# Optimization experiments

Hardware: AMD Instinct MI355X
Metric: run time of the kernel (lower is better)

## Reference

```python
import jax, jax.numpy as jnp
from jax import lax
import numpy as np

C = 768      # embed_dim
H = 8        # num_heads
SR = 2       # sr_ratio
EPS = 1e-5


def setup_inputs() -> dict:
    key = jax.random.key(0)
    ks = jax.random.split(key, 8)
    B, n = 1, 24
    N = n ** 3  # 13824
    s = 0.02
    x = jax.random.normal(ks[0], (B, N, C), jnp.float32)
    wq = jax.random.normal(ks[1], (C, C), jnp.float32) * s          # query (no bias)
    wkv = jax.random.normal(ks[2], (C, 2 * C), jnp.float32) * s     # key_value (no bias)
    sr_w = jax.random.normal(ks[3], (C, C, SR, SR, SR), jnp.float32) * s  # Conv3d OIDHW
    sr_b = jax.random.normal(ks[4], (C,), jnp.float32) * s
    ln_g = jnp.ones((C,), jnp.float32)
    ln_b = jnp.zeros((C,), jnp.float32)
    proj_w = jax.random.normal(ks[5], (C, C), jnp.float32) * s
    proj_b = jax.random.normal(ks[6], (C,), jnp.float32) * s
    return {"x": x, "wq": wq, "wkv": wkv, "sr_w": sr_w, "sr_b": sr_b,
            "ln_g": ln_g, "ln_b": ln_b, "proj_w": proj_w, "proj_b": proj_b}


def reference(x, wq, wkv, sr_w, sr_b, ln_g, ln_b, proj_w, proj_b):
    B, N, Cdim = x.shape
    d = Cdim // H
    n = round(N ** (1.0 / 3.0))
    # q: [B,H,N,d]
    q = (x @ wq).reshape(B, N, H, d).transpose(0, 2, 1, 3)
    # spatial reduction: conv3d with kernel=stride=SR
    x_ = x.transpose(0, 2, 1).reshape(B, Cdim, n, n, n)
    x_ = lax.conv_general_dilated(x_, sr_w, (SR, SR, SR), 'VALID',
                                  dimension_numbers=('NCDHW', 'OIDHW', 'NCDHW'))
    x_ = x_ + sr_b[None, :, None, None, None]
    x_ = x_.reshape(B, Cdim, -1).transpose(0, 2, 1)  # [B, N', C]
    mu = x_.mean(-1, keepdims=True)
    var = x_.var(-1, keepdims=True)
    x_ = (x_ - mu) / jnp.sqrt(var + EPS) * ln_g + ln_b
    # kv: [2,B,H,N',d]
    kv = (x_ @ wkv).reshape(B, -1, 2, H, d).transpose(2, 0, 3, 1, 4)
    k, v = kv[0], kv[1]
    # NOTE: original scales by sqrt(num_heads), not sqrt(head_dim) -- kept faithfully.
    scores = jnp.einsum('bhqd,bhkd->bhqk', q, k) / jnp.sqrt(jnp.float32(H))
    probs = jax.nn.softmax(scores, axis=-1)
    out = jnp.einsum('bhqk,bhkd->bhqd', probs, v)
    out = out.transpose(0, 2, 1, 3).reshape(B, N, Cdim)
    return out @ proj_w + proj_b
```

## Files before the change

kernel.cpp:

```cpp
#include <hip/hip_runtime.h>
#include <hip/hip_bf16.h>

typedef __hip_bfloat16 bf16;
typedef unsigned short u16;

#define CD 768
#define HH 8
#define HD 96
#define NT 13824
#define NR 1728
#define KCONV 6144
#define NRCD 1327104L

typedef __attribute__((ext_vector_type(8))) __bf16 bf16x8;
typedef __attribute__((ext_vector_type(8))) unsigned short us8;
typedef __attribute__((ext_vector_type(4))) unsigned short us4;
typedef __attribute__((ext_vector_type(4))) float floatx4;

#define OFF_XB   0L
#define OFF_Q    21233664L
#define OFF_XR   42467328L
#define OFF_XLN  47775744L
#define OFF_WQT  50429952L
#define OFF_WKVT 51609600L
#define OFF_PRJT 53968896L
#define OFF_SRWR 55148544L
#define OFF_PRB  64587264L

__device__ __forceinline__ float b2f(bf16 v) { return __bfloat162float(v); }
__device__ __forceinline__ floatx4 mfma16(bf16x8 a, bf16x8 b, floatx4 c) {
    return __builtin_amdgcn_mfma_f32_16x16x32_bf16(a, b, c, 0, 0, 0);
}
__device__ __forceinline__ u16 f2bf_bits(float x) {
    return __builtin_bit_cast(u16, __float2bfloat16(x));
}
__device__ __forceinline__ float ldin(const void* p, long i, int bf) {
    return bf ? b2f(((const bf16*)p)[i]) : ((const float*)p)[i];
}
__device__ __forceinline__ int probe_bf(const void* lng) {
    return ((const u16*)lng)[0] == 0x3F80;
}

#define GLOAD16(gp, lp) __builtin_amdgcn_global_load_lds( \
    (const __attribute__((address_space(1))) unsigned int*)(gp), \
    (__attribute__((address_space(3))) unsigned int*)(lp), 16, 0, 0)

__device__ __forceinline__ void do_trans(
    const void* __restrict__ src, bf16* __restrict__ dst, int R, int Cc,
    int bf, int bx32, int by32, int tx, int ty, float (*tile)[33])
{
    const int bx = bx32 * 32, by = by32 * 32;
#pragma unroll
    for (int rr = 0; rr < 4; ++rr)
        tile[ty + rr * 8][tx] = ldin(src, (long)(by + ty + rr * 8) * Cc + bx + tx, bf);
    __syncthreads();
#pragma unroll
    for (int rr = 0; rr < 4; ++rr)
        dst[(long)(bx + ty + rr * 8) * R + by + tx] =
            __float2bfloat16(tile[tx][ty + rr * 8]);
}

__global__ __launch_bounds__(256) void prep_kernel(
    const void* __restrict__ wq, const void* __restrict__ wkv,
    const void* __restrict__ proj_w, const void* __restrict__ sr_w,
    const void* __restrict__ proj_b, const void* __restrict__ x,
    const void* __restrict__ lng,
    bf16* __restrict__ wqT, bf16* __restrict__ wkvT, bf16* __restrict__ prjT,
    bf16* __restrict__ srwR, bf16* __restrict__ prbB, bf16* __restrict__ xb)
{
    __shared__ float tile[32][33];
    const int bf = probe_bf(lng);
    const int tx = threadIdx.x & 31, ty = threadIdx.x >> 5;
    const int id = blockIdx.x;
    if (id < 576) {
        do_trans(wq, wqT, CD, CD, bf, id % 24, id / 24, tx, ty, tile);
    } else if (id < 1728) {
        int j = id - 576;
        do_trans(wkv, wkvT, CD, 1536, bf, j % 48, j / 48, tx, ty, tile);
    } else if (id < 2304) {
        int j = id - 1728;
        do_trans(proj_w, prjT, CD, CD, bf, j % 24, j / 24, tx, ty, tile);
    } else if (id < 3456) {
        int j = id - 2304;
        const long total = 768L * 6144;
        for (long e = (long)j * 256 + threadIdx.x; e < total; e += 1152L * 256) {
            long o = e / 6144;
            int rem = (int)(e - o * 6144);
            int tap = rem / 768, i = rem - tap * 768;
            srwR[e] = __float2bfloat16(ldin(sr_w, o * 6144 + i * 8 + tap, bf));
        }
    } else if (id == 3456) {
        if (threadIdx.x < 96) {
            long c = threadIdx.x;
            if (bf) {
                ((us8*)prbB)[c] = ((const us8*)proj_b)[c];
            } else {
                const float* s = (const float*)proj_b + c * 8;
                us8 o;
#pragma unroll
                for (int jj = 0; jj < 8; ++jj) o[jj] = f2bf_bits(s[jj]);
                ((us8*)prbB)[c] = o;
            }
        }
    } else {
        long c = (long)(id - 3457) * 256 + threadIdx.x;
        if (c < (long)NT * CD / 8) {
            if (bf) {
                ((us8*)xb)[c] = ((const us8*)x)[c];
            } else {
                const float* s = (const float*)x + c * 8;
                us8 o;
#pragma unroll
                for (int jj = 0; jj < 8; ++jj) o[jj] = f2bf_bits(s[jj]);
                ((us8*)xb)[c] = o;
            }
        }
    }
}

template <bool GATHER, bool BIAS, int DST, int SPLITK, bool PRESCALE>
__device__ __forceinline__ void gemm_body(
    const bf16* __restrict__ A, const bf16* __restrict__ Bt,
    const bf16* __restrict__ bias, void* __restrict__ C, bf16* __restrict__ C2,
    int M, int N, int K, const void* __restrict__ lng,
    int bidx, int bidy, int bidz,
    u16 (*__restrict__ Al)[128][32], u16 (*__restrict__ Bl)[128][32])
{
    const int tid  = threadIdx.x;
    const int wave = tid >> 6, lane = tid & 63;
    const int l15  = lane & 15, quad = lane >> 4;
    const int m0 = bidy * 128, n0 = bidx * 128;
    const int mw = (wave & 1) * 64, nw = (wave >> 1) * 64;

    const int row0 = wave * 16 + (lane >> 2);
    const int row1 = row0 + 64;
    const int cb8  = (((lane & 3) ^ ((lane >> 3) & 3)) << 3);

    int tokbase0 = 0, tokbase1 = 0;
    long arow0 = 0, arow1 = 0;
    {
        int mc0 = min(m0 + row0, M - 1);
        int mc1 = min(m0 + row1, M - 1);
        if (GATHER) {
            int zo0 = mc0 / 144, yo0 = (mc0 / 12) % 12, xo0 = mc0 % 12;
            tokbase0 = zo0 * 1152 + yo0 * 48 + xo0 * 2;
            int zo1 = mc1 / 144, yo1 = (mc1 / 12) % 12, xo1 = mc1 % 12;
            tokbase1 = zo1 * 1152 + yo1 * 48 + xo1 * 2;
        } else {
            arow0 = (long)mc0 * K;
            arow1 = (long)mc1 * K;
        }
    }
    const long brow0 = (long)(n0 + row0) * K;
    const long brow1 = (long)(n0 + row1) * K;

    floatx4 acc[4][4];
#pragma unroll
    for (int mi = 0; mi < 4; ++mi)
#pragma unroll
        for (int ni = 0; ni < 4; ++ni) acc[mi][ni] = (floatx4){0.f, 0.f, 0.f, 0.f};

    const int ksteps = K >> 5;
    const int kchunk = ksteps / SPLITK;
    const int kb0 = (SPLITK > 1) ? bidz * kchunk : 0;
    const int kbend = kb0 + kchunk;

    auto stage = [&](int kb, int c) {
        const long ko = (long)kb << 5;
        const bf16 *ga0, *ga1;
        if (GATHER) {
            int kk0 = kb << 5;
            int tap = kk0 / 768;
            int i0  = kk0 - tap * 768 + cb8;
            int toff = (tap >> 2) * 576 + ((tap >> 1) & 1) * 24 + (tap & 1);
            ga0 = A + (long)(tokbase0 + toff) * 768 + i0;
            ga1 = A + (long)(tokbase1 + toff) * 768 + i0;
        } else {
            ga0 = A + arow0 + ko + cb8;
            ga1 = A + arow1 + ko + cb8;
        }
        GLOAD16(ga0, &Al[c][wave * 16][0]);
        GLOAD16(ga1, &Al[c][64 + wave * 16][0]);
        GLOAD16(Bt + brow0 + ko + cb8, &Bl[c][wave * 16][0]);
        GLOAD16(Bt + brow1 + ko + cb8, &Bl[c][64 + wave * 16][0]);
    };

    stage(kb0, 0);
    stage(kb0 + 1, 1);

    const int sl = ((quad ^ ((l15 >> 1) & 3)) << 3);

    for (int kb = kb0; kb < kbend; ++kb) {
        const int cur = (kb - kb0) % 3;
        if (kb + 1 < kbend) asm volatile("s_waitcnt vmcnt(4)" ::: "memory");
        else                asm volatile("s_waitcnt vmcnt(0)" ::: "memory");
        __builtin_amdgcn_s_barrier();
        __builtin_amdgcn_sched_barrier(0);
        if (kb + 2 < kbend) stage(kb + 2, (cur + 2) % 3);

        bf16x8 af[4], bfr[4];
#pragma unroll
        for (int mi = 0; mi < 4; ++mi)
            af[mi] = *(const bf16x8*)&Al[cur][mw + mi * 16 + l15][sl];
#pragma unroll
        for (int ni = 0; ni < 4; ++ni)
            bfr[ni] = *(const bf16x8*)&Bl[cur][nw + ni * 16 + l15][sl];
#pragma unroll
        for (int mi = 0; mi < 4; ++mi)
#pragma unroll
            for (int ni = 0; ni < 4; ++ni)
                acc[mi][ni] = mfma16(af[mi], bfr[ni], acc[mi][ni]);
    }

    const int bf = (DST == 0) ? probe_bf(lng) : 0;

#pragma unroll
    for (int mi = 0; mi < 4; ++mi) {
        int rowb = m0 + mw + mi * 16 + quad * 4;
#pragma unroll
        for (int ni = 0; ni < 4; ++ni) {
            int col = n0 + nw + ni * 16 + l15;
            float bv = BIAS ? b2f(bias[col]) : 0.f;
#pragma unroll
            for (int r = 0; r < 4; ++r) {
                int row = rowb + r;
                if (row < M) {
                    float v = acc[mi][ni][r] + bv;
                    if (PRESCALE) v *= 0.35355339059327373f;
                    long idx = (long)row * N + col;
                    if (DST == 2)      ((float*)C)[idx] = v;
                    else if (DST == 1) ((bf16*)C)[idx] = __float2bfloat16(v);
                    else if (DST == 3) {
                        if (col < 768) ((bf16*)C)[(long)row * 768 + col] = __float2bfloat16(v);
                        else           C2[(long)(col - 768) * NR + row] = __float2bfloat16(v);
                    } else if (DST == 5) {
                        ((float*)C)[(long)bidz * NRCD + idx] = v;
                    } else {
                        if (bf) ((bf16*)C)[idx] = __float2bfloat16(v);
                        else    ((float*)C)[idx] = v;
                    }
                }
            }
        }
    }
}

template <bool GATHER, bool BIAS, int DST, int SPLITK, bool PRESCALE>
__global__ __launch_bounds__(256) void gemm_mfma(
    const bf16* __restrict__ A, const bf16* __restrict__ Bt,
    const bf16* __restrict__ bias, void* __restrict__ C, bf16* __restrict__ C2,
    int M, int N, int K, const void* __restrict__ lng)
{
    __shared__ alignas(16) u16 Al[3][128][32];
    __shared__ alignas(16) u16 Bl[3][128][32];
    gemm_body<GATHER, BIAS, DST, SPLITK, PRESCALE>(
        A, Bt, bias, C, C2, M, N, K, lng,
        blockIdx.x, blockIdx.y, blockIdx.z, Al, Bl);
}

__global__ __launch_bounds__(256) void fused_kv_q_kernel(
    const bf16* __restrict__ Xln, const bf16* __restrict__ wkvT,
    bf16* __restrict__ Kg, bf16* __restrict__ VTg,
    const bf16* __restrict__ xb, const bf16* __restrict__ wqT,
    bf16* __restrict__ Q, const void* __restrict__ lng)
{
    __shared__ alignas(16) u16 Al[3][128][32];
    __shared__ alignas(16) u16 Bl[3][128][32];
    const int id = blockIdx.x;
    if (id < 168) {
        gemm_body<false, false, 3, 1, false>(
            Xln, wkvT, nullptr, Kg, VTg, NR, 1536, CD, lng,
            id % 12, id / 12, 0, Al, Bl);
    } else {
        const int j = id - 168;
        gemm_body<false, false, 1, 1, true>(
            xb, wqT, nullptr, Q, nullptr, NT, CD, CD, lng,
            j % 6, j / 6, 0, Al, Bl);
    }
}

__global__ __launch_bounds__(256) void ln_kernel(
    const float* __restrict__ Xr, const void* __restrict__ srb,
    const void* __restrict__ g, const void* __restrict__ b,
    bf16* __restrict__ Xln)
{
    const int bf = probe_bf(g);
    __shared__ float red[256];
    __shared__ float mu_s, rs_s;
    const int t = blockIdx.x, tid = threadIdx.x;
    const float* row = Xr + (long)t * CD;
    float v0 = (row[tid]              + row[NRCD + tid])
             + (row[2 * NRCD + tid]   + row[3 * NRCD + tid])       + ldin(srb, tid, bf);
    float v1 = (row[tid + 256]        + row[NRCD + tid + 256])
             + (row[2 * NRCD + tid + 256] + row[3 * NRCD + tid + 256]) + ldin(srb, tid + 256, bf);
    float v2 = (row[tid + 512]        + row[NRCD + tid + 512])
             + (row[2 * NRCD + tid + 512] + row[3 * NRCD + tid + 512]) + ldin(srb, tid + 512, bf);
    red[tid] = v0 + v1 + v2;
    __syncthreads();
    for (int off = 128; off; off >>= 1) {
        if (tid < off) red[tid] += red[tid + off];
        __syncthreads();
    }
    if (tid == 0) mu_s = red[0] * (1.0f / CD);
    __syncthreads();
    float mu = mu_s;
    float d0 = v0 - mu, d1 = v1 - mu, d2 = v2 - mu;
    red[tid] = d0 * d0 + d1 * d1 + d2 * d2;
    __syncthreads();
    for (int off = 128; off; off >>= 1) {
        if (tid < off) red[tid] += red[tid + off];
        __syncthreads();
    }
    if (tid == 0) rs_s = rsqrtf(red[0] * (1.0f / CD) + 1e-5f);
    __syncthreads();
    float rs = rs_s;
    bf16* orow = Xln + (long)t * CD;
    orow[tid]       = __float2bfloat16(d0 * rs * ldin(g, tid, bf)       + ldin(b, tid, bf));
    orow[tid + 256] = __float2bfloat16(d1 * rs * ldin(g, tid + 256, bf) + ldin(b, tid + 256, bf));
    orow[tid + 512] = __float2bfloat16(d2 * rs * ldin(g, tid + 512, bf) + ldin(b, tid + 512, bf));
}

__global__ __launch_bounds__(256, 2) void attn_mfma_kernel(
    const bf16* __restrict__ Qg, const bf16* __restrict__ Kg,
    const bf16* __restrict__ VTg, bf16* __restrict__ Og)
{
    __shared__ u16 Ks[64][104];
    __shared__ u16 Vt[96][72];
    __shared__ u16 PT[4][64][64];

    const int tid  = threadIdx.x;
    const int wave = tid >> 6;
    const int lane = tid & 63;
    const int l15  = lane & 15;
    const int quad = lane >> 4;

    const int lin  = blockIdx.y * 54 + blockIdx.x;
    const int nid  = (lin & 7) * 54 + (lin >> 3);
    const int h    = nid / 54;
    const int qblk = nid - h * 54;
    const int q0   = qblk * 256 + wave * 64;

    bf16x8 bq[4][3];
#pragma unroll
    for (int qc = 0; qc < 4; ++qc)
#pragma unroll
        for (int kc = 0; kc < 3; ++kc)
            bq[qc][kc] = *(const bf16x8*)(Qg + (long)(q0 + qc * 16 + l15) * CD
                                          + h * HD + kc * 32 + quad * 8);

    floatx4 o[4][6];
    float lp[4] = {0.f, 0.f, 0.f, 0.f};
#pragma unroll
    for (int qc = 0; qc < 4; ++qc)
#pragma unroll
        for (int dc = 0; dc < 6; ++dc) o[qc][dc] = (floatx4){0.f, 0.f, 0.f, 0.f};

    const int stok = tid >> 2;
    const int dseg = (tid & 3) * 24;
    const int vdim = tid >> 3;
    const int vt8  = (tid & 7) << 3;
    const u16* kbase = (const u16*)Kg + (long)stok * 768 + h * HD + dseg;
    const u16* vbase = (const u16*)VTg + (long)(h * HD + vdim) * NR + vt8;

    us8 kreg[3], vreg[3];
#pragma unroll
    for (int s = 0; s < 3; ++s) kreg[s] = *(const us8*)(kbase + s * 8);
#pragma unroll
    for (int i = 0; i < 3; ++i) vreg[i] = *(const us8*)(vbase + (long)i * 32 * NR);

    for (int kt = 0; kt < NR; kt += 64) {
        __syncthreads();
#pragma unroll
        for (int s = 0; s < 3; ++s) *(us8*)&Ks[stok][dseg + s * 8] = kreg[s];
#pragma unroll
        for (int i = 0; i < 3; ++i) *(us8*)&Vt[vdim + i * 32][vt8] = vreg[i];
        __syncthreads();

        if (kt + 64 < NR) {
            const u16* k2 = kbase + (long)(kt + 64) * 768;
            const u16* v2 = vbase + (kt + 64);
#pragma unroll
            for (int s = 0; s < 3; ++s) kreg[s] = *(const us8*)(k2 + s * 8);
#pragma unroll
            for (int i = 0; i < 3; ++i) vreg[i] = *(const us8*)(v2 + (long)i * 32 * NR);
        }

#pragma unroll
        for (int tc = 0; tc < 4; ++tc) {
            bf16x8 ak[3];
#pragma unroll
            for (int kc = 0; kc < 3; ++kc)
                ak[kc] = *(const bf16x8*)&Ks[tc * 16 + l15][kc * 32 + quad * 8];
#pragma unroll
            for (int qc = 0; qc < 4; ++qc) {
                floatx4 acc = {0.f, 0.f, 0.f, 0.f};
                __builtin_amdgcn_s_setprio(1);
#pragma unroll
                for (int kc = 0; kc < 3; ++kc) acc = mfma16(ak[kc], bq[qc][kc], acc);
                __builtin_amdgcn_s_setprio(0);
                float e0 = __expf(acc[0]), e1 = __expf(acc[1]);
                float e2 = __expf(acc[2]), e3 = __expf(acc[3]);
                lp[qc] += (e0 + e1) + (e2 + e3);
                us4 p4;
                p4[0] = f2bf_bits(e0); p4[1] = f2bf_bits(e1);
                p4[2] = f2bf_bits(e2); p4[3] = f2bf_bits(e3);
                const int pb = (tc * 2 + (quad >> 1)) ^ (l15 & 7);
                *(us4*)&PT[wave][qc * 16 + l15][pb * 8 + (quad & 1) * 4] = p4;
            }
        }

#pragma unroll
        for (int ks = 0; ks < 2; ++ks) {
            bf16x8 ap[4];
#pragma unroll
            for (int qc = 0; qc < 4; ++qc) {
                const int rb = (ks * 4 + quad) ^ (l15 & 7);
                ap[qc] = *(const bf16x8*)&PT[wave][qc * 16 + l15][rb * 8];
            }
            __builtin_amdgcn_s_setprio(1);
#pragma unroll
            for (int dc = 0; dc < 6; ++dc) {
                bf16x8 bv = *(const bf16x8*)&Vt[dc * 16 + l15][ks * 32 + quad * 8];
#pragma unroll
                for (int qc = 0; qc < 4; ++qc)
                    o[qc][dc] = mfma16(ap[qc], bv, o[qc][dc]);
            }
            __builtin_amdgcn_s_setprio(0);
        }
    }

#pragma unroll
    for (int qc = 0; qc < 4; ++qc) {
        float ls = lp[qc];
        ls += __shfl_xor(ls, 16);
        ls += __shfl_xor(ls, 32);
        float inv = 1.0f / ls;
#pragma unroll
        for (int r = 0; r < 4; ++r) {
            float invr = __shfl(inv, quad * 4 + r, 16);
            int row = q0 + qc * 16 + quad * 4 + r;
#pragma unroll
            for (int dc = 0; dc < 6; ++dc)
                Og[(long)row * CD + h * HD + dc * 16 + l15] =
                    __float2bfloat16(o[qc][dc][r] * invr);
        }
    }
}

extern "C" void kernel_launch(void* const* d_in, const int* in_sizes, int n_in,
                              void* d_out, int out_size, void* d_ws, size_t ws_size,
                              hipStream_t stream) {
    const void* x      = d_in[0];
    const void* wq     = d_in[1];
    const void* wkv    = d_in[2];
    const void* sr_w   = d_in[3];
    const void* sr_b   = d_in[4];
    const void* ln_g   = d_in[5];
    const void* ln_b   = d_in[6];
    const void* proj_w = d_in[7];
    const void* proj_b = d_in[8];

    char* ws = (char*)d_ws;
    bf16*  xb    = (bf16*)(ws + OFF_XB);
    bf16*  O     = (bf16*)(ws + OFF_XB);
    float* Xr4   = (float*)(ws + OFF_Q);
    bf16*  Q     = (bf16*)(ws + OFF_Q);
    bf16*  Kg    = (bf16*)(ws + OFF_XR);
    bf16*  VTg   = (bf16*)(ws + OFF_XR + 2654208);
    bf16*  Xln   = (bf16*)(ws + OFF_XLN);
    bf16*  wqT   = (bf16*)(ws + OFF_WQT);
    bf16*  wkvT  = (bf16*)(ws + OFF_WKVT);
    bf16*  prjT  = (bf16*)(ws + OFF_PRJT);
    bf16*  srwR  = (bf16*)(ws + OFF_SRWR);
    bf16*  prbB  = (bf16*)(ws + OFF_PRB);

    prep_kernel<<<8641, 256, 0, stream>>>(wq, wkv, proj_w, sr_w, proj_b, x,
                                          ln_g, wqT, wkvT, prjT, srwR, prbB, xb);

    gemm_mfma<true, false, 5, 4, false><<<dim3(6, 14, 4), 256, 0, stream>>>(
        xb, srwR, nullptr, Xr4, nullptr, NR, CD, KCONV, ln_g);
    ln_kernel<<<NR, 256, 0, stream>>>(Xr4, sr_b, ln_g, ln_b, Xln);
    fused_kv_q_kernel<<<816, 256, 0, stream>>>(Xln, wkvT, Kg, VTg,
                                               xb, wqT, Q, ln_g);
    attn_mfma_kernel<<<dim3(NT / 256, HH), 256, 0, stream>>>(Q, Kg, VTg, O);
    gemm_mfma<false, true, 0, 1, false><<<dim3(6, 108), 256, 0, stream>>>(
        O, prjT, prbB, d_out, nullptr, NT, CD, CD, ln_g);
}
```

Baseline: 359.9 us.

## Remap GEMM block order for XCD locality and cut conv split-K from 4 to 3

Adds a block-index remap, (id&7)*stride + (id>>3), to the fused KV/Q GEMM and to a new 1-D proj kernel. Consecutive tiles then land on the same XCD, which should improve L2 reuse of the A/B panels across MI355X's chiplets. It also lowers the conv split-K factor from 4 to 3 and changes the LayerNorm reduction to sum three partials. That cuts fp32 partial traffic, but each conv block now runs a longer K loop with fewer blocks in the grid.

```diff
diff --git a/kernel.cpp b/kernel.cpp
--- a/kernel.cpp
+++ b/kernel.cpp
@@ -268,15 +268,31 @@
     __shared__ alignas(16) u16 Bl[3][128][32];
     const int id = blockIdx.x;
     if (id < 168) {
+        const int nid = (id & 7) * 21 + (id >> 3);
         gemm_body<false, false, 3, 1, false>(
             Xln, wkvT, nullptr, Kg, VTg, NR, 1536, CD, lng,
-            id % 12, id / 12, 0, Al, Bl);
+            nid % 12, nid / 12, 0, Al, Bl);
     } else {
         const int j = id - 168;
+        const int nid = (j & 7) * 81 + (j >> 3);
         gemm_body<false, false, 1, 1, true>(
             xb, wqT, nullptr, Q, nullptr, NT, CD, CD, lng,
-            j % 6, j / 6, 0, Al, Bl);
-    }
+            nid % 6, nid / 6, 0, Al, Bl);
+    }
+}
+
+__global__ __launch_bounds__(256) void proj_kernel(
+    const bf16* __restrict__ O, const bf16* __restrict__ prjT,
+    const bf16* __restrict__ prbB, void* __restrict__ out,
+    const void* __restrict__ lng)
+{
+    __shared__ alignas(16) u16 Al[3][128][32];
+    __shared__ alignas(16) u16 Bl[3][128][32];
+    const int lin = blockIdx.x;
+    const int nid = (lin & 7) * 81 + (lin >> 3);
+    gemm_body<false, true, 0, 1, false>(
+        O, prjT, prbB, out, nullptr, NT, CD, CD, lng,
+        nid % 6, nid / 6, 0, Al, Bl);
 }
 
 __global__ __launch_bounds__(256) void ln_kernel(
@@ -289,12 +305,12 @@
     __shared__ float mu_s, rs_s;
     const int t = blockIdx.x, tid = threadIdx.x;
     const float* row = Xr + (long)t * CD;
-    float v0 = (row[tid]              + row[NRCD + tid])
-             + (row[2 * NRCD + tid]   + row[3 * NRCD + tid])       + ldin(srb, tid, bf);
-    float v1 = (row[tid + 256]        + row[NRCD + tid + 256])
-             + (row[2 * NRCD + tid + 256] + row[3 * NRCD + tid + 256]) + ldin(srb, tid + 256, bf);
-    float v2 = (row[tid + 512]        + row[NRCD + tid + 512])
-             + (row[2 * NRCD + tid + 512] + row[3 * NRCD + tid + 512]) + ldin(srb, tid + 512, bf);
+    float v0 = (row[tid]       + row[NRCD + tid])
+             + row[2 * NRCD + tid]       + ldin(srb, tid, bf);
+    float v1 = (row[tid + 256] + row[NRCD + tid + 256])
+             + row[2 * NRCD + tid + 256] + ldin(srb, tid + 256, bf);
+    float v2 = (row[tid + 512] + row[NRCD + tid + 512])
+             + row[2 * NRCD + tid + 512] + ldin(srb, tid + 512, bf);
     red[tid] = v0 + v1 + v2;
     __syncthreads();
     for (int off = 128; off; off >>= 1) {
@@ -463,7 +479,7 @@
     char* ws = (char*)d_ws;
     bf16*  xb    = (bf16*)(ws + OFF_XB);
     bf16*  O     = (bf16*)(ws + OFF_XB);
-    float* Xr4   = (float*)(ws + OFF_Q);
+    float* Xr3   = (float*)(ws + OFF_Q);
     bf16*  Q     = (bf16*)(ws + OFF_Q);
     bf16*  Kg    = (bf16*)(ws + OFF_XR);
     bf16*  VTg   = (bf16*)(ws + OFF_XR + 2654208);
@@ -477,12 +493,11 @@
     prep_kernel<<<8641, 256, 0, stream>>>(wq, wkv, proj_w, sr_w, proj_b, x,
                                           ln_g, wqT, wkvT, prjT, srwR, prbB, xb);
 
-    gemm_mfma<true, false, 5, 4, false><<<dim3(6, 14, 4), 256, 0, stream>>>(
-        xb, srwR, nullptr, Xr4, nullptr, NR, CD, KCONV, ln_g);
-    ln_kernel<<<NR, 256, 0, stream>>>(Xr4, sr_b, ln_g, ln_b, Xln);
+    gemm_mfma<true, false, 5, 3, false><<<dim3(6, 14, 3), 256, 0, stream>>>(
+        xb, srwR, nullptr, Xr3, nullptr, NR, CD, KCONV, ln_g);
+    ln_kernel<<<NR, 256, 0, stream>>>(Xr3, sr_b, ln_g, ln_b, Xln);
     fused_kv_q_kernel<<<816, 256, 0, stream>>>(Xln, wkvT, Kg, VTg,
                                                xb, wqT, Q, ln_g);
     attn_mfma_kernel<<<dim3(NT / 256, HH), 256, 0, stream>>>(Q, Kg, VTg, O);
-    gemm_mfma<false, true, 0, 1, false><<<dim3(6, 108), 256, 0, stream>>>(
-        O, prjT, prbB, d_out, nullptr, NT, CD, CD, ln_g);
-}
+    proj_kernel<<<648, 256, 0, stream>>>(O, prjT, prbB, d_out, ln_g);
+}
```

After: 381.0 us. 5.9% more time.
